# Performance work log

Measured on AMD Instinct MI355X. Metric: run time of the kernel, lower is better.

The kernel has to match this reference:

```python
import jax, jax.numpy as jnp
import numpy as np

N_HEAD = 4
N_FEAT = 256
D_K = N_FEAT // N_HEAD
MAX_SEQ_LEN = 500
LN_EPS = 1e-6


def setup_inputs() -> dict:
    key = jax.random.key(0)
    ks = jax.random.split(key, 12)
    B, L, F = 64, 500, N_FEAT
    s = lambda fan_in: 1.0 / np.sqrt(fan_in)
    return {
        "q": jax.random.normal(ks[0], (B, L, F), jnp.float32),
        "k": jax.random.normal(ks[1], (B, L, F), jnp.float32),
        "v": jax.random.normal(ks[2], (B, L, F), jnp.float32),
        # weights stored as [in, out] (torch Linear transposed)
        "w_qs": jax.random.normal(ks[3], (F, F), jnp.float32) * s(F),
        "w_vs": jax.random.normal(ks[4], (F, F), jnp.float32) * s(F),
        "w1": jax.random.normal(ks[5], (D_K, D_K), jnp.float32) * s(D_K),
        "b1": jax.random.normal(ks[6], (D_K,), jnp.float32) * s(D_K),
        "w2": jax.random.normal(ks[7], (D_K, MAX_SEQ_LEN), jnp.float32) * s(D_K),
        "b2": jax.random.normal(ks[8], (MAX_SEQ_LEN,), jnp.float32) * s(D_K),
        "fc_w": jax.random.normal(ks[9], (F, F), jnp.float32) * s(F),
        "ln_g": jnp.ones((F,), jnp.float32),
        "ln_b": jnp.zeros((F,), jnp.float32),
    }


def reference(q, k, v, w_qs, w_vs, w1, b1, w2, b2, fc_w, ln_g, ln_b):
    B, L, F = q.shape
    H, dk = N_HEAD, D_K
    residual = q
    # head projections -> [B, H, L, dk]
    qh = (q @ w_qs).reshape(B, L, H, dk).transpose(0, 2, 1, 3)
    vh = (v @ w_vs).reshape(B, L, H, dk).transpose(0, 2, 1, 3)
    # dense synthesizer: relu(q W1 + b1) W2 + b2, slice to len_q
    weight = jax.nn.relu(qh @ w1 + b1)
    attn = (weight @ w2 + b2)[..., :L]            # [B, H, L, L]
    attn = jax.nn.softmax(attn, axis=-1)
    out = attn @ vh                                # [B, H, L, dk]
    out = out.transpose(0, 2, 1, 3).reshape(B, L, F)
    out = out @ fc_w + residual
    # LayerNorm(eps=1e-6)
    mu = jnp.mean(out, axis=-1, keepdims=True)
    var = jnp.var(out, axis=-1, keepdims=True)
    out = (out - mu) * jax.lax.rsqrt(var + LN_EPS) * ln_g + ln_b
    return out
```

## Files before the change

kernel.cpp:

```cpp
#include <hip/hip_runtime.h>
#include <math.h>

#define B_   64
#define L_   500
#define F_   256
#define H_   4
#define DK   64

typedef unsigned short u16;
typedef unsigned int   u32;
typedef __attribute__((ext_vector_type(8))) short short8;
typedef __attribute__((ext_vector_type(4))) float f32x4;

static __device__ __forceinline__ u16 f2bf(float f) {
    u32 u = __float_as_uint(f);
    u32 r = (u + 0x7FFFu + ((u >> 16) & 1u)) >> 16;
    return (u16)r;
}
static __device__ __forceinline__ u16 f2bf_up(float f) {
    return (u16)((__float_as_uint(f) + 0x8000u) >> 16);
}

typedef __attribute__((address_space(3))) u32 lds32;
typedef const __attribute__((address_space(1))) u32 gbl32;
static __device__ __forceinline__ void gload_lds16(const u16* g, u16* l) {
    __builtin_amdgcn_global_load_lds((gbl32*)g, (lds32*)l, 16, 0, 0);
}

__global__ __launch_bounds__(256) void prep_kernel(
    const float* __restrict__ wq, const float* __restrict__ wv,
    const float* __restrict__ fcw, const float* __restrict__ w1,
    const float* __restrict__ w2, const float* __restrict__ b2,
    u16* __restrict__ wqT, u16* __restrict__ wvT, u16* __restrict__ fcwT,
    u16* __restrict__ w1T, u16* __restrict__ w2sw,
    u16* __restrict__ qh_bf, u16* __restrict__ vhT, float* __restrict__ b2p)
{
    int t = blockIdx.x * 256 + threadIdx.x;
    int stride = gridDim.x * 256;
    for (int i = t; i < 256 * 256; i += stride) {
        int n = i >> 8, k = i & 255;
        wqT[i]  = f2bf(wq[k * 256 + n]);
        wvT[i]  = f2bf(wv[k * 256 + n]);
        fcwT[i] = f2bf(fcw[k * 256 + n]);
    }
    for (int i = t; i < 64 * 64; i += stride) {
        int n = i >> 6, k = i & 63;
        w1T[i] = f2bf(w1[k * 64 + n]);
    }
    for (int i = t; i < 512 * 64; i += stride) {
        int cc  = i >> 12;
        int row = (i >> 6) & 63;
        int kc  = i & 63;
        int n   = cc * 64 + row;
        int kl  = kc ^ ((row & 7) << 3);
        w2sw[i] = f2bf(n < 500 ? w2[kl * 500 + n] : 0.f);
    }
    for (int i = t; i < 512; i += stride)
        b2p[i] = (i < 500) ? b2[i] : -1e30f;
    for (int i = t; i < 3072; i += stride)
        qh_bf[8192000 + i] = 0;
    for (int i = t; i < 196608; i += stride) {
        int bh = i / 768;
        int r  = i - bh * 768;
        int d  = r / 12;
        int kk = 52 + (r - d * 12);
        vhT[((size_t)((bh * 8 + 7) * 64 + d)) * 64 + (kk ^ ((d & 7) << 3))] = 0;
    }
}

__global__ __launch_bounds__(512) void proj_kernel(
    const float* __restrict__ q, const float* __restrict__ v,
    const u16* __restrict__ wqT, const u16* __restrict__ wvT,
    u16* __restrict__ qh_bf, u16* __restrict__ vhT)
{
    const int which = blockIdx.y;
    const float* __restrict__ x = which ? v : q;
    const u16*   __restrict__ wT = which ? wvT : wqT;

    __shared__ u16 Xs[64][72];
    __shared__ u16 Ws[256][72];

    const int tid  = threadIdx.x;
    const int wvid = tid >> 6, ln = tid & 63;
    const int n16  = ln & 15, quad = ln >> 4;
    const int wr   = wvid >> 2, wc = wvid & 3;
    const int row0 = blockIdx.x * 64;

    f32x4 acc[2][4];
    #pragma unroll
    for (int mt = 0; mt < 2; mt++)
        #pragma unroll
        for (int nt = 0; nt < 4; nt++) acc[mt][nt] = (f32x4){0.f, 0.f, 0.f, 0.f};

    for (int kc = 0; kc < 256; kc += 64) {
        #pragma unroll
        for (int j = 0; j < 2; j++) {
            int idx = tid + 512 * j;
            int m = idx >> 4, k4 = idx & 15;
            float4 a = *(const float4*)&x[(size_t)(row0 + m) * 256 + kc + k4 * 4];
            __align__(8) u16 t4[4] = {f2bf(a.x), f2bf(a.y), f2bf(a.z), f2bf(a.w)};
            *(uint2*)&Xs[m][k4 * 4] = *(const uint2*)t4;
        }
        #pragma unroll
        for (int j = 0; j < 4; j++) {
            int idx = tid + 512 * j;
            int n = idx >> 3, k8 = idx & 7;
            *(uint4*)&Ws[n][k8 * 8] = *(const uint4*)&wT[n * 256 + kc + k8 * 8];
        }
        __syncthreads();
        #pragma unroll
        for (int ks = 0; ks < 2; ks++) {
            short8 af[2], bfr[4];
            #pragma unroll
            for (int mt = 0; mt < 2; mt++)
                af[mt] = *(const short8*)&Xs[wr * 32 + mt * 16 + n16][ks * 32 + quad * 8];
            #pragma unroll
            for (int nt = 0; nt < 4; nt++)
                bfr[nt] = *(const short8*)&Ws[wc * 64 + nt * 16 + n16][ks * 32 + quad * 8];
            #pragma unroll
            for (int mt = 0; mt < 2; mt++)
                #pragma unroll
                for (int nt = 0; nt < 4; nt++)
                    acc[mt][nt] = __builtin_amdgcn_mfma_f32_16x16x32_bf16(
                        af[mt], bfr[nt], acc[mt][nt], 0, 0, 0);
        }
        __syncthreads();
    }

    if (which == 0) {
        #pragma unroll
        for (int mt = 0; mt < 2; mt++) {
            int m0 = row0 + wr * 32 + mt * 16 + quad * 4;
            int b  = m0 / 500;
            int l0 = m0 - 500 * b;
            #pragma unroll
            for (int nt = 0; nt < 4; nt++) {
                int d = nt * 16 + n16;
                u16* dst = qh_bf + ((size_t)((b * 4 + wc) * 500 + l0)) * 64 + d;
                #pragma unroll
                for (int i = 0; i < 4; i++)
                    dst[(size_t)i * 64] = f2bf(acc[mt][nt][i]);
            }
        }
    } else {
        #pragma unroll
        for (int mt = 0; mt < 2; mt++) {
            int m0 = row0 + wr * 32 + mt * 16 + quad * 4;
            int b  = m0 / 500;
            int l0 = m0 - 500 * b;
            int cc = l0 >> 6, kk = l0 & 63;
            #pragma unroll
            for (int nt = 0; nt < 4; nt++) {
                int d = nt * 16 + n16;
                __align__(8) u16 t4[4];
                #pragma unroll
                for (int i = 0; i < 4; i++) t4[i] = f2bf(acc[mt][nt][i]);
                size_t base = ((size_t)(((b * 4 + wc) * 8 + cc) * 64 + d)) * 64;
                *(uint2*)&vhT[base + (kk ^ ((d & 7) << 3))] = *(const uint2*)t4;
            }
        }
    }
}

__global__ __launch_bounds__(512, 2) void attn_kernel(
    const u16* __restrict__ qh, const u16* __restrict__ vhT,
    const u16* __restrict__ w1T, const float* __restrict__ b1,
    const u16* __restrict__ w2sw, const float* __restrict__ b2p,
    u16* __restrict__ ctx)
{
    __shared__ __align__(16) u16 w2all[32768];
    __shared__ __align__(16) u16 vall[32768];
    __shared__ __align__(16) float b2s[512];
    __shared__ __align__(16) u16 scr[8][16][72];

    const int tid  = threadIdx.x;
    const int wv   = tid >> 6;
    const int ln   = tid & 63;
    const int n16  = ln & 15;
    const int quad = ln >> 4;
    const int bh   = blockIdx.x;

    const u16* vg = vhT + (size_t)bh * 32768;

    short8 a0[4], a1[4];
    #pragma unroll
    for (int rg = 0; rg < 4; rg++) {
        const u16* qbase = qh + ((size_t)(bh * 500 + rg * 128 + wv * 16 + n16)) * 64;
        a0[rg] = *(const short8*)(qbase + quad * 8);
        a1[rg] = *(const short8*)(qbase + 32 + quad * 8);
    }
    short8 w1b0[4], w1b1[4];
    float  b1v[4];
    #pragma unroll
    for (int nt = 0; nt < 4; nt++) {
        const u16* wb = w1T + (nt * 16 + n16) * 64;
        w1b0[nt] = *(const short8*)(wb + quad * 8);
        w1b1[nt] = *(const short8*)(wb + 32 + quad * 8);
        b1v[nt]  = b1[nt * 16 + n16];
    }
    __builtin_amdgcn_sched_barrier(0);

    {
        int base = wv * 4096;
        #pragma unroll
        for (int j = 0; j < 8; j++)
            gload_lds16(w2sw + base + j * 512 + ln * 8, &w2all[base + j * 512]);
        #pragma unroll
        for (int j = 0; j < 8; j++)
            gload_lds16(vg + base + j * 512 + ln * 8, &vall[base + j * 512]);
        if (wv < 2)
            gload_lds16((const u16*)b2p + wv * 512 + ln * 8, (u16*)&b2s[wv * 256]);
    }
    __builtin_amdgcn_sched_barrier(0);

    short8 sa0[4], sa1[4];
    #pragma unroll
    for (int rg = 0; rg < 4; rg++) {
        #pragma unroll
        for (int nt = 0; nt < 4; nt++) {
            float bias = b1v[nt];
            f32x4 c = {bias, bias, bias, bias};
            c = __builtin_amdgcn_mfma_f32_16x16x32_bf16(a0[rg], w1b0[nt], c, 0, 0, 0);
            c = __builtin_amdgcn_mfma_f32_16x16x32_bf16(a1[rg], w1b1[nt], c, 0, 0, 0);
            int col = nt * 16 + n16;
            #pragma unroll
            for (int i = 0; i < 4; i++)
                scr[wv][quad * 4 + i][col] = f2bf(fmaxf(c[i], 0.f));
        }
        sa0[rg] = *(const short8*)&scr[wv][n16][quad * 8];
        sa1[rg] = *(const short8*)&scr[wv][n16][32 + quad * 8];
    }

    __syncthreads();

    const int b = bh >> 2, h = bh & 3;
    #pragma unroll
    for (int rg = 0; rg < 4; rg++) {
        f32x4 oacc[4];
        #pragma unroll
        for (int nt = 0; nt < 4; nt++) oacc[nt] = (f32x4){0.f, 0.f, 0.f, 0.f};
        float sm[4] = {0.f, 0.f, 0.f, 0.f};

        #pragma unroll 2
        for (int cc = 0; cc < 8; cc++) {
            f32x4 c8[4];
            #pragma unroll
            for (int t = 0; t < 4; t++) {
                int r  = t * 16 + n16;
                int sw = (r & 7) << 3;
                const u16* wb = &w2all[cc * 4096 + r * 64];
                short8 b0  = *(const short8*)&wb[(quad * 8) ^ sw];
                short8 b1f = *(const short8*)&wb[(32 + quad * 8) ^ sw];
                float bias = b2s[cc * 64 + r];
                f32x4 c = {bias, bias, bias, bias};
                c = __builtin_amdgcn_mfma_f32_16x16x32_bf16(sa0[rg], b0, c, 0, 0, 0);
                c = __builtin_amdgcn_mfma_f32_16x16x32_bf16(sa1[rg], b1f, c, 0, 0, 0);
                c8[t] = c;
            }
            #pragma unroll
            for (int t = 0; t < 4; t++) {
                int col = t * 16 + n16;
                #pragma unroll
                for (int i = 0; i < 4; i++) {
                    float e = __expf(c8[t][i]);
                    sm[i] += e;
                    scr[wv][quad * 4 + i][col] = f2bf_up(e);
                }
            }
            #pragma unroll
            for (int ks = 0; ks < 2; ks++) {
                short8 pa = *(const short8*)&scr[wv][n16][ks * 32 + quad * 8];
                #pragma unroll
                for (int nt = 0; nt < 4; nt++) {
                    int d   = nt * 16 + n16;
                    int swd = (d & 7) << 3;
                    short8 vb2 = *(const short8*)&vall[cc * 4096 + d * 64 +
                                                       ((ks * 32 + quad * 8) ^ swd)];
                    oacc[nt] = __builtin_amdgcn_mfma_f32_16x16x32_bf16(
                        pa, vb2, oacc[nt], 0, 0, 0);
                }
            }
        }

        #pragma unroll
        for (int off = 1; off < 16; off <<= 1) {
            #pragma unroll
            for (int i = 0; i < 4; i++) sm[i] += __shfl_xor(sm[i], off);
        }
        #pragma unroll
        for (int i = 0; i < 4; i++) {
            int lrow = rg * 128 + wv * 16 + quad * 4 + i;
            if (lrow < 500) {
                float s = 1.f / sm[i];
                u16* dst = &ctx[((size_t)(b * 500 + lrow)) * 256 + h * 64];
                #pragma unroll
                for (int nt = 0; nt < 4; nt++)
                    dst[nt * 16 + n16] = f2bf(oacc[nt][i] * s);
            }
        }
    }
}

__global__ __launch_bounds__(512) void final_kernel(
    const u16* __restrict__ ctx, const u16* __restrict__ fcwT,
    const float* __restrict__ qres, const float* __restrict__ g,
    const float* __restrict__ bta, float* __restrict__ out)
{
    __shared__ u16 Xs[64][72];
    __shared__ u16 Ws[256][72];
    __shared__ float red[4][2][64];
    __shared__ float murs[2][64];

    const int tid  = threadIdx.x;
    const int wvid = tid >> 6, ln = tid & 63;
    const int n16  = ln & 15, quad = ln >> 4;
    const int wr   = wvid >> 2, wc = wvid & 3;
    const int row0 = blockIdx.x * 64;

    f32x4 acc[2][4];
    #pragma unroll
    for (int mt = 0; mt < 2; mt++)
        #pragma unroll
        for (int nt = 0; nt < 4; nt++) acc[mt][nt] = (f32x4){0.f, 0.f, 0.f, 0.f};

    for (int kc = 0; kc < 256; kc += 64) {
        {
            int idx = tid;
            int m = idx >> 3, k8 = idx & 7;
            *(uint4*)&Xs[m][k8 * 8] =
                *(const uint4*)&ctx[(size_t)(row0 + m) * 256 + kc + k8 * 8];
        }
        #pragma unroll
        for (int j = 0; j < 4; j++) {
            int idx = tid + 512 * j;
            int n = idx >> 3, k8 = idx & 7;
            *(uint4*)&Ws[n][k8 * 8] = *(const uint4*)&fcwT[n * 256 + kc + k8 * 8];
        }
        __syncthreads();
        #pragma unroll
        for (int ks = 0; ks < 2; ks++) {
            short8 af[2], bfr[4];
            #pragma unroll
            for (int mt = 0; mt < 2; mt++)
                af[mt] = *(const short8*)&Xs[wr * 32 + mt * 16 + n16][ks * 32 + quad * 8];
            #pragma unroll
            for (int nt = 0; nt < 4; nt++)
                bfr[nt] = *(const short8*)&Ws[wc * 64 + nt * 16 + n16][ks * 32 + quad * 8];
            #pragma unroll
            for (int mt = 0; mt < 2; mt++)
                #pragma unroll
                for (int nt = 0; nt < 4; nt++)
                    acc[mt][nt] = __builtin_amdgcn_mfma_f32_16x16x32_bf16(
                        af[mt], bfr[nt], acc[mt][nt], 0, 0, 0);
        }
        __syncthreads();
    }

    #pragma unroll
    for (int mt = 0; mt < 2; mt++) {
        int m0 = row0 + wr * 32 + mt * 16 + quad * 4;
        #pragma unroll
        for (int i = 0; i < 4; i++) {
            const float* rp = &qres[(size_t)(m0 + i) * 256 + wc * 64 + n16];
            #pragma unroll
            for (int nt = 0; nt < 4; nt++)
                acc[mt][nt][i] += rp[nt * 16];
        }
    }
    #pragma unroll
    for (int mt = 0; mt < 2; mt++) {
        #pragma unroll
        for (int i = 0; i < 4; i++) {
            float s1 = 0.f, s2 = 0.f;
            #pragma unroll
            for (int nt = 0; nt < 4; nt++) {
                float vv = acc[mt][nt][i];
                s1 += vv; s2 += vv * vv;
            }
            #pragma unroll
            for (int off = 1; off < 16; off <<= 1) {
                s1 += __shfl_xor(s1, off);
                s2 += __shfl_xor(s2, off);
            }
            if (n16 == 0) {
                int r = wr * 32 + mt * 16 + quad * 4 + i;
                red[wc][0][r] = s1;
                red[wc][1][r] = s2;
            }
        }
    }
    __syncthreads();
    if (tid < 64) {
        float S1 = red[0][0][tid] + red[1][0][tid] + red[2][0][tid] + red[3][0][tid];
        float S2 = red[0][1][tid] + red[1][1][tid] + red[2][1][tid] + red[3][1][tid];
        float mu  = S1 * 0.00390625f;
        float var = S2 * 0.00390625f - mu * mu;
        murs[0][tid] = mu;
        murs[1][tid] = rsqrtf(var + 1e-6f);
    }
    __syncthreads();

    float gv[4], bv[4];
    #pragma unroll
    for (int nt = 0; nt < 4; nt++) {
        int col = wc * 64 + nt * 16 + n16;
        gv[nt] = g[col];
        bv[nt] = bta[col];
    }
    #pragma unroll
    for (int mt = 0; mt < 2; mt++) {
        int rb = wr * 32 + mt * 16 + quad * 4;
        #pragma unroll
        for (int i = 0; i < 4; i++) {
            float mu = murs[0][rb + i];
            float rs = murs[1][rb + i];
            float* op = &out[(size_t)(row0 + rb + i) * 256 + wc * 64 + n16];
            #pragma unroll
            for (int nt = 0; nt < 4; nt++)
                op[nt * 16] = (acc[mt][nt][i] - mu) * rs * gv[nt] + bv[nt];
        }
    }
}

extern "C" void kernel_launch(void* const* d_in, const int* in_sizes, int n_in,
                              void* d_out, int out_size, void* d_ws, size_t ws_size,
                              hipStream_t stream)
{
    const float* q   = (const float*)d_in[0];
    const float* v   = (const float*)d_in[2];
    const float* wqs = (const float*)d_in[3];
    const float* wvs = (const float*)d_in[4];
    const float* w1  = (const float*)d_in[5];
    const float* b1  = (const float*)d_in[6];
    const float* w2  = (const float*)d_in[7];
    const float* b2  = (const float*)d_in[8];
    const float* fcw = (const float*)d_in[9];
    const float* lng = (const float*)d_in[10];
    const float* lnb = (const float*)d_in[11];
    float* out = (float*)d_out;

    u16* qh_bf = (u16*)d_ws;
    u16* vhT   = qh_bf + 8200192;
    u16* w1T   = vhT + 8388608;
    u16* w2sw  = w1T + 4096;
    u16* wqT   = w2sw + 32768;
    u16* wvT   = wqT + 65536;
    u16* fcwT  = wvT + 65536;
    u16* ctx   = fcwT + 65536;
    float* b2p = (float*)(qh_bf + 8195072);

    prep_kernel <<<dim3(64),     256, 0, stream>>>(wqs, wvs, fcw, w1, w2, b2,
                                                   wqT, wvT, fcwT, w1T, w2sw,
                                                   qh_bf, vhT, b2p);
    proj_kernel <<<dim3(500, 2), 512, 0, stream>>>(q, v, wqT, wvT, qh_bf, vhT);
    attn_kernel <<<dim3(256),    512, 0, stream>>>(qh_bf, vhT, w1T, b1, w2sw, b2p, ctx);
    final_kernel<<<dim3(500),    512, 0, stream>>>(ctx, fcwT, q, lng, lnb, out);
}
```

Measured before the change: 91.33 us.

## Double-buffer V chunks in attention kernel and double block size to 1024 threads

The attention kernel now runs 16 waves per block, each handling 2 row groups instead of 4. It streams V through a two-slot LDS ring, prefetching the next 4096-element chunk while the current one is used, instead of loading all of V up front. The aim is to cut the LDS footprint, hide V load latency and raise the number of waves per block. In exchange it adds a __syncthreads per chunk, and the 1024-thread launch bound may limit registers per thread. The prefetch issued in each iteration is not explicitly waited on (no vmcnt wait) before the next iteration reads that buffer, so correctness depends on the barrier ordering the loads.

Measured after the change: 122.1 us. 33.7% more time.

```diff
diff --git a/kernel.cpp b/kernel.cpp
--- a/kernel.cpp
+++ b/kernel.cpp
@@ -162,16 +162,16 @@
     }
 }
 
-__global__ __launch_bounds__(512, 2) void attn_kernel(
+__global__ __launch_bounds__(1024) void attn_kernel(
     const u16* __restrict__ qh, const u16* __restrict__ vhT,
     const u16* __restrict__ w1T, const float* __restrict__ b1,
     const u16* __restrict__ w2sw, const float* __restrict__ b2p,
     u16* __restrict__ ctx)
 {
     __shared__ __align__(16) u16 w2all[32768];
-    __shared__ __align__(16) u16 vall[32768];
+    __shared__ __align__(16) u16 v_s[2][4096];
     __shared__ __align__(16) float b2s[512];
-    __shared__ __align__(16) u16 scr[8][16][72];
+    __shared__ __align__(16) u16 scr[16][16][72];
 
     const int tid  = threadIdx.x;
     const int wv   = tid >> 6;
@@ -182,10 +182,10 @@
 
     const u16* vg = vhT + (size_t)bh * 32768;
 
-    short8 a0[4], a1[4];
-    #pragma unroll
-    for (int rg = 0; rg < 4; rg++) {
-        const u16* qbase = qh + ((size_t)(bh * 500 + rg * 128 + wv * 16 + n16)) * 64;
+    short8 a0[2], a1[2];
+    #pragma unroll
+    for (int rg = 0; rg < 2; rg++) {
+        const u16* qbase = qh + ((size_t)(bh * 500 + rg * 256 + wv * 16 + n16)) * 64;
         a0[rg] = *(const short8*)(qbase + quad * 8);
         a1[rg] = *(const short8*)(qbase + 32 + quad * 8);
     }
@@ -201,21 +201,21 @@
     __builtin_amdgcn_sched_barrier(0);
 
     {
-        int base = wv * 4096;
-        #pragma unroll
-        for (int j = 0; j < 8; j++)
+        int base = wv * 2048;
+        #pragma unroll
+        for (int j = 0; j < 4; j++)
             gload_lds16(w2sw + base + j * 512 + ln * 8, &w2all[base + j * 512]);
-        #pragma unroll
-        for (int j = 0; j < 8; j++)
-            gload_lds16(vg + base + j * 512 + ln * 8, &vall[base + j * 512]);
-        if (wv < 2)
-            gload_lds16((const u16*)b2p + wv * 512 + ln * 8, (u16*)&b2s[wv * 256]);
+        if (wv < 8)
+            gload_lds16(vg + wv * 512 + ln * 8, &v_s[0][wv * 512]);
+        if (wv >= 14)
+            gload_lds16((const u16*)b2p + (wv - 14) * 512 + ln * 8,
+                        (u16*)&b2s[(wv - 14) * 256]);
     }
     __builtin_amdgcn_sched_barrier(0);
 
-    short8 sa0[4], sa1[4];
-    #pragma unroll
-    for (int rg = 0; rg < 4; rg++) {
+    short8 sa0[2], sa1[2];
+    #pragma unroll
+    for (int rg = 0; rg < 2; rg++) {
         #pragma unroll
         for (int nt = 0; nt < 4; nt++) {
             float bias = b1v[nt];
@@ -231,18 +231,24 @@
         sa1[rg] = *(const short8*)&scr[wv][n16][32 + quad * 8];
     }
 
+    f32x4 oacc[2][4];
+    #pragma unroll
+    for (int rg = 0; rg < 2; rg++)
+        #pragma unroll
+        for (int nt = 0; nt < 4; nt++) oacc[rg][nt] = (f32x4){0.f, 0.f, 0.f, 0.f};
+    float sm[2][4] = {{0.f, 0.f, 0.f, 0.f}, {0.f, 0.f, 0.f, 0.f}};
+
     __syncthreads();
 
-    const int b = bh >> 2, h = bh & 3;
-    #pragma unroll
-    for (int rg = 0; rg < 4; rg++) {
-        f32x4 oacc[4];
-        #pragma unroll
-        for (int nt = 0; nt < 4; nt++) oacc[nt] = (f32x4){0.f, 0.f, 0.f, 0.f};
-        float sm[4] = {0.f, 0.f, 0.f, 0.f};
-
-        #pragma unroll 2
-        for (int cc = 0; cc < 8; cc++) {
+    #pragma unroll 2
+    for (int cc = 0; cc < 8; cc++) {
+        if (cc < 7 && wv < 8)
+            gload_lds16(vg + (cc + 1) * 4096 + wv * 512 + ln * 8,
+                        &v_s[(cc + 1) & 1][wv * 512]);
+        const u16* vbuf = &v_s[cc & 1][0];
+
+        #pragma unroll
+        for (int rg = 0; rg < 2; rg++) {
             f32x4 c8[4];
             #pragma unroll
             for (int t = 0; t < 4; t++) {
@@ -263,7 +269,7 @@
                 #pragma unroll
                 for (int i = 0; i < 4; i++) {
                     float e = __expf(c8[t][i]);
-                    sm[i] += e;
+                    sm[rg][i] += e;
                     scr[wv][quad * 4 + i][col] = f2bf_up(e);
                 }
             }
@@ -274,28 +280,33 @@
                 for (int nt = 0; nt < 4; nt++) {
                     int d   = nt * 16 + n16;
                     int swd = (d & 7) << 3;
-                    short8 vb2 = *(const short8*)&vall[cc * 4096 + d * 64 +
+                    short8 vb2 = *(const short8*)&vbuf[d * 64 +
                                                        ((ks * 32 + quad * 8) ^ swd)];
-                    oacc[nt] = __builtin_amdgcn_mfma_f32_16x16x32_bf16(
-                        pa, vb2, oacc[nt], 0, 0, 0);
+                    oacc[rg][nt] = __builtin_amdgcn_mfma_f32_16x16x32_bf16(
+                        pa, vb2, oacc[rg][nt], 0, 0, 0);
                 }
             }
         }
-
+        __syncthreads();
+    }
+
+    const int b = bh >> 2, h = bh & 3;
+    #pragma unroll
+    for (int rg = 0; rg < 2; rg++) {
         #pragma unroll
         for (int off = 1; off < 16; off <<= 1) {
             #pragma unroll
-            for (int i = 0; i < 4; i++) sm[i] += __shfl_xor(sm[i], off);
+            for (int i = 0; i < 4; i++) sm[rg][i] += __shfl_xor(sm[rg][i], off);
         }
         #pragma unroll
         for (int i = 0; i < 4; i++) {
-            int lrow = rg * 128 + wv * 16 + quad * 4 + i;
+            int lrow = rg * 256 + wv * 16 + quad * 4 + i;
             if (lrow < 500) {
-                float s = 1.f / sm[i];
+                float s = 1.f / sm[rg][i];
                 u16* dst = &ctx[((size_t)(b * 500 + lrow)) * 256 + h * 64];
                 #pragma unroll
                 for (int nt = 0; nt < 4; nt++)
-                    dst[nt * 16 + n16] = f2bf(oacc[nt][i] * s);
+                    dst[nt * 16 + n16] = f2bf(oacc[rg][nt][i] * s);
             }
         }
     }
@@ -453,6 +464,6 @@
                                                    wqT, wvT, fcwT, w1T, w2sw,
                                                    qh_bf, vhT, b2p);
     proj_kernel <<<dim3(500, 2), 512, 0, stream>>>(q, v, wqT, wvT, qh_bf, vhT);
-    attn_kernel <<<dim3(256),    512, 0, stream>>>(qh_bf, vhT, w1T, b1, w2sw, b2p, ctx);
+    attn_kernel <<<dim3(256),   1024, 0, stream>>>(qh_bf, vhT, w1T, b1, w2sw, b2p, ctx);
     final_kernel<<<dim3(500),    512, 0, stream>>>(ctx, fcwT, q, lng, lnb, out);
 }
```
